# Performance work log

Measured on AMD Instinct MI355X. Metric: run time of the kernel, lower is better.

Reference implementation:

```python
import jax, jax.numpy as jnp
import numpy as np

EPS = 1e-8
ELASTICITY = jnp.array([0.05, 0.12, 0.08, 0.15, 0.10], dtype=jnp.float32)
N_SIDE = 3  # sqrt(control_points=9)


def _kernel_distance(d2):
    # kornia TPS radial basis: 0.5 * r^2 * log(r^2 + eps)
    return 0.5 * d2 * jnp.log(d2 + EPS)


def _pair_sq_dist(a, b):  # [B,N,2],[B,M,2] -> [B,N,M]
    return jnp.sum((a[:, :, None, :] - b[:, None, :, :]) ** 2, axis=-1)


def grid_sample_bilinear(img, grid):
    """F.grid_sample, mode=bilinear, padding_mode=zeros, align_corners=True.
    img [B,C,H,W], grid [B,H,W,2] with (x,y) in [-1,1]."""
    B, C, H, W = img.shape
    gx = (grid[..., 0] + 1.0) * 0.5 * (W - 1)
    gy = (grid[..., 1] + 1.0) * 0.5 * (H - 1)
    x0 = jnp.floor(gx); y0 = jnp.floor(gy)
    x1 = x0 + 1.0; y1 = y0 + 1.0
    wx1 = gx - x0; wx0 = 1.0 - wx1
    wy1 = gy - y0; wy0 = 1.0 - wy1
    b = jnp.arange(B)[:, None, None]

    def gather(yi, xi):
        valid = (xi >= 0) & (xi <= W - 1) & (yi >= 0) & (yi <= H - 1)
        xc = jnp.clip(xi, 0, W - 1).astype(jnp.int32)
        yc = jnp.clip(yi, 0, H - 1).astype(jnp.int32)
        v = img[b, :, yc, xc]  # [B,H,W,C]
        return v * valid[..., None].astype(img.dtype)

    out = (gather(y0, x0) * (wy0 * wx0)[..., None]
           + gather(y0, x1) * (wy0 * wx1)[..., None]
           + gather(y1, x0) * (wy1 * wx0)[..., None]
           + gather(y1, x1) * (wy1 * wx1)[..., None])
    return jnp.transpose(out, (0, 3, 1, 2))


def control_points_src(B):
    ii, jj = jnp.meshgrid(jnp.arange(N_SIDE, dtype=jnp.float32),
                          jnp.arange(N_SIDE, dtype=jnp.float32), indexing='ij')
    src = jnp.stack([2.0 * ii / (N_SIDE - 1) - 1.0,
                     2.0 * jj / (N_SIDE - 1) - 1.0], axis=-1).reshape(-1, 2)
    return jnp.broadcast_to(src, (B, N_SIDE * N_SIDE, 2))


def point_elasticity(masks_f):
    # masks_f [B,nc,H,W]; 5x5 window around each control point, argmax class
    H, W = masks_f.shape[2], masks_f.shape[3]
    elas = []
    for i in range(N_SIDE):
        for j in range(N_SIDE):
            y = int(i / (N_SIDE - 1) * (H - 1))
            x = int(j / (N_SIDE - 1) * (W - 1))
            y0, y1 = max(0, y - 2), min(H, y + 3)
            x0, x1 = max(0, x - 2), min(W, x + 3)
            region = masks_f[:, :, y0:y1, x0:x1].sum((2, 3))  # [B,nc]
            dom = jnp.argmax(region, axis=1)
            elas.append(ELASTICITY[dom])
    return jnp.stack(elas, axis=1)  # [B,9]


def get_tps_transform(src, dst):
    B, N, _ = src.shape
    K = _kernel_distance(_pair_sq_dist(src, src))                 # [B,N,N]
    P = jnp.concatenate([jnp.ones((B, N, 1), src.dtype), src], -1)  # [B,N,3]
    top = jnp.concatenate([K, P], axis=-1)
    bot = jnp.concatenate([jnp.swapaxes(P, 1, 2),
                           jnp.zeros((B, 3, 3), src.dtype)], axis=-1)
    L = jnp.concatenate([top, bot], axis=1)                        # [B,N+3,N+3]
    rhs = jnp.concatenate([dst, jnp.zeros((B, 3, 2), src.dtype)], axis=1)
    w = jnp.linalg.solve(L, rhs)
    return w[:, :N], w[:, N:]


def warp_image_tps(img, centers, kernel_w, affine_w):
    B, C, H, W = img.shape
    gx, gy = jnp.meshgrid(jnp.linspace(-1.0, 1.0, W), jnp.linspace(-1.0, 1.0, H))
    pts = jnp.stack([gx.ravel(), gy.ravel()], axis=-1)             # [HW,2]
    pts = jnp.broadcast_to(pts, (B, H * W, 2))
    k = _kernel_distance(_pair_sq_dist(pts, centers))              # [B,HW,N]
    pts_aug = jnp.concatenate([jnp.ones((B, H * W, 1), img.dtype), pts], -1)
    warped = k @ kernel_w + pts_aug @ affine_w                     # [B,HW,2]
    return grid_sample_bilinear(img, warped.reshape(B, H, W, 2))


def tps_transform(img, masks_f, noise):
    B = img.shape[0]
    disp = noise * point_elasticity(masks_f)[..., None]            # [B,9,2]
    # smooth the single interior control point (i=j=1 -> idx 4)
    neigh = (disp[:, 1] + disp[:, 7] + disp[:, 3] + disp[:, 5]) * 0.25
    disp = disp.at[:, 4].set(0.8 * disp[:, 4] + 0.2 * neigh)
    src = control_points_src(B)
    kw, aw = get_tps_transform(src, src + disp)
    return warp_image_tps(img, src, kw, aw)


def class_aware_mixup(x, masks_f, lam, perm):
    bg = (masks_f.sum(1, keepdims=True) == 0).astype(x.dtype)
    fg = (masks_f == 1).astype(x.dtype).sum(1, keepdims=True)
    return bg * x + fg * (lam * x + (1.0 - lam) * x[perm])


def setup_inputs() -> dict:
    key = jax.random.key(0)
    k1, k2, k3, k4, k5, k6 = jax.random.split(key, 6)
    B, H, W, NC = 128, 192, 192, 5
    return {
        'x': jax.random.normal(k1, (B, 1, H, W), dtype=jnp.float32),
        'masks': jax.random.randint(k2, (B, NC, H, W), 0, 2, dtype=jnp.int32),
        'lam': jax.random.beta(k3, 0.4, 0.4, dtype=jnp.float32),
        'perm': jax.random.permutation(k4, B).astype(jnp.int32),
        'noise_g': jax.random.normal(k5, (B, 9, 2), dtype=jnp.float32),
        'noise_l': jax.random.normal(k6, (B, 9, 2), dtype=jnp.float32),
        'epoch': 10,
        'total_epochs': 100,
    }


def reference(x, masks, lam, perm, noise_g, noise_l, epoch, total_epochs):
    masks_f = masks.astype(x.dtype)
    mixed_x = class_aware_mixup(x, masks_f, lam, perm)
    global_aug = tps_transform(mixed_x, masks_f, noise_g)
    local_aug = tps_transform(x, masks_f, noise_l)
    return (global_aug, local_aug)
```

## Files before the change

kernel.cpp:

```cpp
#include <hip/hip_runtime.h>
#include <math.h>

#define B_    128
#define H_    192
#define W_    192
#define NC_   5
#define HW_   (H_*W_)
#define NPTS  9
#define EPS_  1e-8f
#define CHUNK 8
#define MIXB  (B_*HW_/4/256)
#define LOCB  ((W_/64)*(H_/4)*(B_/CHUNK))

typedef int   vint4   __attribute__((ext_vector_type(4)));
typedef float vfloat4 __attribute__((ext_vector_type(4)));
typedef float vfloat2 __attribute__((ext_vector_type(2)));

struct LinvT { float m[12][NPTS]; };

__global__ void prep_kernel(const int* __restrict__ masks,
                            const float* __restrict__ ng,
                            const float* __restrict__ nl,
                            LinvT Linv, float* __restrict__ wts)
{
    const float ETAB[5] = {0.05f, 0.12f, 0.08f, 0.15f, 0.1f};
    __shared__ int   sums[NPTS][NC_];
    __shared__ float elas_s[NPTS];
    int b = blockIdx.x;
    int t = threadIdx.x;

    if (t < NPTS * NC_) {
        int pt = t / NC_, c = t - pt * NC_;
        int i = pt / 3, j = pt % 3;
        int yc = (i * (H_ - 1)) / 2;
        int xc = (j * (W_ - 1)) / 2;
        int y0 = yc - 2 < 0 ? 0 : yc - 2;
        int y1 = yc + 3 > H_ ? H_ : yc + 3;
        int x0 = xc - 2 < 0 ? 0 : xc - 2;
        int x1 = xc + 3 > W_ ? W_ : xc + 3;
        int s = 0;
        for (int y = y0; y < y1; ++y)
            for (int xx = x0; xx < x1; ++xx)
                s += masks[((size_t)b * NC_ + c) * HW_ + y * W_ + xx];
        sums[pt][c] = s;
    }
    __syncthreads();
    if (t < NPTS) {
        int best = -1, best_c = 0;
        #pragma unroll
        for (int c = 0; c < NC_; ++c) {
            int s = sums[t][c];
            if (s > best) { best = s; best_c = c; }
        }
        elas_s[t] = ETAB[best_c];
    }
    __syncthreads();
    if (t < 24) {
        int tr = t / 12, r = t - tr * 12;
        const float* noise = (tr == 0) ? ng : nl;
        float disp[NPTS][2];
        #pragma unroll
        for (int k = 0; k < NPTS; ++k) {
            float e = elas_s[k];
            disp[k][0] = noise[((size_t)b * NPTS + k) * 2 + 0] * e;
            disp[k][1] = noise[((size_t)b * NPTS + k) * 2 + 1] * e;
        }
        #pragma unroll
        for (int c = 0; c < 2; ++c) {
            float nb = (disp[1][c] + disp[7][c] + disp[3][c] + disp[5][c]) * 0.25f;
            disp[4][c] = 0.8f * disp[4][c] + 0.2f * nb;
        }
        float a0 = 0.f, a1 = 0.f;
        #pragma unroll
        for (int k = 0; k < NPTS; ++k) {
            float d0 = (float)(k / 3 - 1) + disp[k][0];
            float d1 = (float)(k % 3 - 1) + disp[k][1];
            a0 += Linv.m[r][k] * d0;
            a1 += Linv.m[r][k] * d1;
        }
        float* wout = wts + ((size_t)tr * B_ + b) * 24;
        wout[r * 2 + 0] = a0;
        wout[r * 2 + 1] = a1;
    }
}

__device__ __forceinline__ void tps_coords_pk(
    const vfloat2* __restrict__ wt2, float px, float py, const float* __restrict__ u,
    int& o00, int& o01, int& o10, int& o11,
    float& w00, float& w01, float& w10, float& w11)
{
    vfloat2 g = wt2[9];
    g = __builtin_elementwise_fma((vfloat2){px, px}, wt2[10], g);
    g = __builtin_elementwise_fma((vfloat2){py, py}, wt2[11], g);
    #pragma unroll
    for (int k = 0; k < NPTS; ++k)
        g = __builtin_elementwise_fma((vfloat2){u[k], u[k]}, wt2[k], g);
    const float sc = 0.5f * (float)(W_ - 1);
    float ix = fmaf(g.x, sc, sc);
    float iy = fmaf(g.y, sc, sc);
    float x0f = floorf(ix), y0f = floorf(iy);
    float wx1 = ix - x0f, wx0 = 1.f - wx1;
    float wy1 = iy - y0f, wy0 = 1.f - wy1;
    int x0 = (int)x0f, y0 = (int)y0f;
    float fx0 = ((unsigned)x0 < 192u)       ? wx0 : 0.f;
    float fx1 = ((unsigned)(x0 + 1) < 192u) ? wx1 : 0.f;
    float fy0 = ((unsigned)y0 < 192u)       ? wy0 : 0.f;
    float fy1 = ((unsigned)(y0 + 1) < 192u) ? wy1 : 0.f;
    w00 = fy0 * fx0; w01 = fy0 * fx1; w10 = fy1 * fx0; w11 = fy1 * fx1;
    int o = y0 * W_ + x0;
    o00 = min(max(o, 0), HW_ - 1);
    o01 = min(max(o + 1, 0), HW_ - 1);
    o10 = min(max(o + W_, 0), HW_ - 1);
    o11 = min(max(o + W_ + 1, 0), HW_ - 1);
}

__device__ __forceinline__ void warp_body(
    const float* __restrict__ srcb, const float* __restrict__ wts,
    float* __restrict__ out, int gx, int gy, int combo0)
{
    int tx  = threadIdx.x;
    int wpx = gx * 64 + (tx & 63);
    int h   = gy * 4 + (tx >> 6);
    int p   = h * W_ + wpx;
    float px = -1.f + wpx * (2.f / (float)(W_ - 1));
    float py = -1.f + h   * (2.f / (float)(H_ - 1));

    float u[NPTS];
    #pragma unroll
    for (int k = 0; k < NPTS; ++k) {
        float dx = px - (float)(k / 3 - 1);
        float dy = py - (float)(k % 3 - 1);
        float d2 = dx * dx + dy * dy;
        u[k] = 0.5f * d2 * __logf(d2 + EPS_);
    }

    const vfloat2* wt2base = reinterpret_cast<const vfloat2*>(wts);

    #pragma unroll
    for (int g4 = 0; g4 < CHUNK; g4 += 4) {
        int   o00[4], o01[4], o10[4], o11[4];
        float w00[4], w01[4], w10[4], w11[4];
        const float* src[4];
        #pragma unroll
        for (int q = 0; q < 4; ++q) {
            int combo = combo0 + g4 + q;
            int b = combo & (B_ - 1);
            src[q] = srcb + (size_t)b * HW_;
            tps_coords_pk(wt2base + (size_t)combo * 12, px, py, u,
                          o00[q], o01[q], o10[q], o11[q],
                          w00[q], w01[q], w10[q], w11[q]);
        }
        float v00[4], v01[4], v10[4], v11[4];
        #pragma unroll
        for (int q = 0; q < 4; ++q) {
            v00[q] = src[q][o00[q]];
            v01[q] = src[q][o01[q]];
            v10[q] = src[q][o10[q]];
            v11[q] = src[q][o11[q]];
        }
        #pragma unroll
        for (int q = 0; q < 4; ++q) {
            int combo = combo0 + g4 + q;
            float val = w00[q] * v00[q] + w01[q] * v01[q] +
                        w10[q] * v10[q] + w11[q] * v11[q];
            __builtin_nontemporal_store(val, &out[(size_t)combo * HW_ + p]);
        }
    }
}

__global__ __launch_bounds__(256, 2) void mix_local_kernel(
    const float* __restrict__ x, const int* __restrict__ masks,
    const float* __restrict__ lam_p, const int* __restrict__ perm,
    float* __restrict__ mixed, const float* __restrict__ wts,
    float* __restrict__ out)
{
    int bid   = blockIdx.x;
    int group = bid / 3;
    int r     = bid - group * 3;

    if (r < 2) {
        int mb  = group * 2 + r;
        int idx = mb * 256 + threadIdx.x;
        float lam = lam_p[0];
        int b  = idx / (HW_ / 4);
        int p4 = (idx - b * (HW_ / 4)) * 4;
        const vfloat4 xv = *reinterpret_cast<const vfloat4*>(x + (size_t)b * HW_ + p4);
        int pb = perm[b];
        const vfloat4 xp = *reinterpret_cast<const vfloat4*>(x + (size_t)pb * HW_ + p4);

        vint4 ma[NC_];
        #pragma unroll
        for (int c = 0; c < NC_; ++c)
            ma[c] = __builtin_nontemporal_load(
                reinterpret_cast<const vint4*>(masks + ((size_t)b * NC_ + c) * HW_ + p4));
        vfloat4 outv;
        #pragma unroll
        for (int l = 0; l < 4; ++l) {
            int s = 0, fg = 0;
            #pragma unroll
            for (int c = 0; c < NC_; ++c) { int m = ma[c][l]; s += m; fg += (m == 1); }
            float bg = (s == 0) ? 1.f : 0.f;
            outv[l] = bg * xv[l] + (float)fg * (lam * xv[l] + (1.f - lam) * xp[l]);
        }
        *reinterpret_cast<vfloat4*>(mixed + (size_t)b * HW_ + p4) = outv;
    } else {
        int lb = group;
        int gx = lb % 3;
        int gy = (lb / 3) % 48;
        int gz = lb / 144;
        warp_body(x, wts, out, gx, gy, B_ + gz * CHUNK);
    }
}

__global__ __launch_bounds__(256, 2) void warp_global_kernel(
    const float* __restrict__ mixed, const float* __restrict__ wts,
    float* __restrict__ out)
{
    warp_body(mixed, wts, out, blockIdx.x, blockIdx.y, blockIdx.z * CHUNK);
}

static void build_linv(LinvT* out)
{
    double srcp[NPTS][2];
    for (int k = 0; k < NPTS; ++k) {
        srcp[k][0] = (double)(k / 3) - 1.0;
        srcp[k][1] = (double)(k % 3) - 1.0;
    }
    double A[12][24];
    for (int r = 0; r < 12; ++r)
        for (int c = 0; c < 24; ++c) A[r][c] = 0.0;
    for (int i = 0; i < NPTS; ++i) {
        for (int j = 0; j < NPTS; ++j) {
            double dx = srcp[i][0] - srcp[j][0];
            double dy = srcp[i][1] - srcp[j][1];
            double d2 = dx * dx + dy * dy;
            A[i][j] = 0.5 * d2 * log(d2 + 1e-8);
        }
        A[i][9]  = 1.0; A[i][10] = srcp[i][0]; A[i][11] = srcp[i][1];
        A[9][i]  = 1.0; A[10][i] = srcp[i][0]; A[11][i] = srcp[i][1];
    }
    for (int r = 0; r < 12; ++r) A[r][12 + r] = 1.0;
    for (int col = 0; col < 12; ++col) {
        int piv = col; double mx = fabs(A[col][col]);
        for (int r = col + 1; r < 12; ++r)
            if (fabs(A[r][col]) > mx) { mx = fabs(A[r][col]); piv = r; }
        if (piv != col)
            for (int c = 0; c < 24; ++c) { double tmp = A[col][c]; A[col][c] = A[piv][c]; A[piv][c] = tmp; }
        double d = A[col][col];
        for (int c = 0; c < 24; ++c) A[col][c] /= d;
        for (int r = 0; r < 12; ++r) {
            if (r == col) continue;
            double f = A[r][col];
            if (f != 0.0)
                for (int c = 0; c < 24; ++c) A[r][c] -= f * A[col][c];
        }
    }
    for (int r = 0; r < 12; ++r)
        for (int k = 0; k < NPTS; ++k)
            out->m[r][k] = (float)A[r][12 + k];
}

extern "C" void kernel_launch(void* const* d_in, const int* in_sizes, int n_in,
                              void* d_out, int out_size, void* d_ws, size_t ws_size,
                              hipStream_t stream)
{
    (void)in_sizes; (void)n_in; (void)out_size; (void)ws_size;
    const float* x     = (const float*)d_in[0];
    const int*   masks = (const int*)d_in[1];
    const float* lam   = (const float*)d_in[2];
    const int*   perm  = (const int*)d_in[3];
    const float* ng    = (const float*)d_in[4];
    const float* nl    = (const float*)d_in[5];
    float* out = (float*)d_out;

    char* ws = (char*)d_ws;
    float* wts   = (float*)ws;
    float* mixed = (float*)(ws + 32768);

    LinvT Linv;
    build_linv(&Linv);

    prep_kernel<<<B_, 64, 0, stream>>>(masks, ng, nl, Linv, wts);
    mix_local_kernel<<<MIXB + LOCB, 256, 0, stream>>>(
        x, masks, lam, perm, mixed, wts, out);
    warp_global_kernel<<<dim3(W_ / 64, H_ / 4, (B_ / CHUNK)), 256, 0, stream>>>(
        mixed, wts, out);
}
```

Before: 58.62 us.

## Split mixup and warps into three staged kernels to overlap global warp

```diff
diff --git a/kernel.cpp b/kernel.cpp
--- a/kernel.cpp
+++ b/kernel.cpp
@@ -9,8 +9,8 @@
 #define NPTS  9
 #define EPS_  1e-8f
 #define CHUNK 8
-#define MIXB  (B_*HW_/4/256)
-#define LOCB  ((W_/64)*(H_/4)*(B_/CHUNK))
+#define MIXBH 2304
+#define LOCBH 1152
 
 typedef int   vint4   __attribute__((ext_vector_type(4)));
 typedef float vfloat4 __attribute__((ext_vector_type(4)));
@@ -168,7 +168,37 @@
     }
 }
 
-__global__ __launch_bounds__(256, 2) void mix_local_kernel(
+__device__ __forceinline__ void mixup_body(
+    const float* __restrict__ x, const int* __restrict__ masks,
+    const float* __restrict__ lam_p, const int* __restrict__ perm,
+    float* __restrict__ mixed, int mb)
+{
+    int idx = mb * 256 + threadIdx.x;
+    float lam = lam_p[0];
+    int b  = idx / (HW_ / 4);
+    int p4 = (idx - b * (HW_ / 4)) * 4;
+    const vfloat4 xv = *reinterpret_cast<const vfloat4*>(x + (size_t)b * HW_ + p4);
+    int pb = perm[b];
+    const vfloat4 xp = *reinterpret_cast<const vfloat4*>(x + (size_t)pb * HW_ + p4);
+
+    vint4 ma[NC_];
+    #pragma unroll
+    for (int c = 0; c < NC_; ++c)
+        ma[c] = __builtin_nontemporal_load(
+            reinterpret_cast<const vint4*>(masks + ((size_t)b * NC_ + c) * HW_ + p4));
+    vfloat4 outv;
+    #pragma unroll
+    for (int l = 0; l < 4; ++l) {
+        int s = 0, fg = 0;
+        #pragma unroll
+        for (int c = 0; c < NC_; ++c) { int m = ma[c][l]; s += m; fg += (m == 1); }
+        float bg = (s == 0) ? 1.f : 0.f;
+        outv[l] = bg * xv[l] + (float)fg * (lam * xv[l] + (1.f - lam) * xp[l]);
+    }
+    *reinterpret_cast<vfloat4*>(mixed + (size_t)b * HW_ + p4) = outv;
+}
+
+__global__ __launch_bounds__(256, 2) void half_a_kernel(
     const float* __restrict__ x, const int* __restrict__ masks,
     const float* __restrict__ lam_p, const int* __restrict__ perm,
     float* __restrict__ mixed, const float* __restrict__ wts,
@@ -177,46 +207,42 @@
     int bid   = blockIdx.x;
     int group = bid / 3;
     int r     = bid - group * 3;
-
     if (r < 2) {
-        int mb  = group * 2 + r;
-        int idx = mb * 256 + threadIdx.x;
-        float lam = lam_p[0];
-        int b  = idx / (HW_ / 4);
-        int p4 = (idx - b * (HW_ / 4)) * 4;
-        const vfloat4 xv = *reinterpret_cast<const vfloat4*>(x + (size_t)b * HW_ + p4);
-        int pb = perm[b];
-        const vfloat4 xp = *reinterpret_cast<const vfloat4*>(x + (size_t)pb * HW_ + p4);
-
-        vint4 ma[NC_];
-        #pragma unroll
-        for (int c = 0; c < NC_; ++c)
-            ma[c] = __builtin_nontemporal_load(
-                reinterpret_cast<const vint4*>(masks + ((size_t)b * NC_ + c) * HW_ + p4));
-        vfloat4 outv;
-        #pragma unroll
-        for (int l = 0; l < 4; ++l) {
-            int s = 0, fg = 0;
-            #pragma unroll
-            for (int c = 0; c < NC_; ++c) { int m = ma[c][l]; s += m; fg += (m == 1); }
-            float bg = (s == 0) ? 1.f : 0.f;
-            outv[l] = bg * xv[l] + (float)fg * (lam * xv[l] + (1.f - lam) * xp[l]);
-        }
-        *reinterpret_cast<vfloat4*>(mixed + (size_t)b * HW_ + p4) = outv;
+        mixup_body(x, masks, lam_p, perm, mixed, group * 2 + r);
     } else {
         int lb = group;
-        int gx = lb % 3;
-        int gy = (lb / 3) % 48;
-        int gz = lb / 144;
+        int gx = lb % 3, gy = (lb / 3) % 48, gz = lb / 144;
         warp_body(x, wts, out, gx, gy, B_ + gz * CHUNK);
     }
 }
 
-__global__ __launch_bounds__(256, 2) void warp_global_kernel(
+__global__ __launch_bounds__(256, 2) void half_b_kernel(
+    const float* __restrict__ x, const int* __restrict__ masks,
+    const float* __restrict__ lam_p, const int* __restrict__ perm,
+    float* __restrict__ mixed, const float* __restrict__ wts,
+    float* __restrict__ out)
+{
+    int bid   = blockIdx.x;
+    int group = bid / 4;
+    int r     = bid - group * 4;
+    if (r < 2) {
+        mixup_body(x, masks, lam_p, perm, mixed, MIXBH + group * 2 + r);
+    } else if (r == 2) {
+        int lb = group;
+        int gx = lb % 3, gy = (lb / 3) % 48, gz = lb / 144;
+        warp_body(x, wts, out, gx, gy, B_ + 64 + gz * CHUNK);
+    } else {
+        int lb = group;
+        int gx = lb % 3, gy = (lb / 3) % 48, gz = lb / 144;
+        warp_body(mixed, wts, out, gx, gy, gz * CHUNK);
+    }
+}
+
+__global__ __launch_bounds__(256, 2) void half_c_kernel(
     const float* __restrict__ mixed, const float* __restrict__ wts,
     float* __restrict__ out)
 {
-    warp_body(mixed, wts, out, blockIdx.x, blockIdx.y, blockIdx.z * CHUNK);
+    warp_body(mixed, wts, out, blockIdx.x, blockIdx.y, 64 + blockIdx.z * CHUNK);
 }
 
 static void build_linv(LinvT* out)
@@ -281,8 +307,9 @@
     build_linv(&Linv);
 
     prep_kernel<<<B_, 64, 0, stream>>>(masks, ng, nl, Linv, wts);
-    mix_local_kernel<<<MIXB + LOCB, 256, 0, stream>>>(
+    half_a_kernel<<<MIXBH + LOCBH, 256, 0, stream>>>(
         x, masks, lam, perm, mixed, wts, out);
-    warp_global_kernel<<<dim3(W_ / 64, H_ / 4, (B_ / CHUNK)), 256, 0, stream>>>(
-        mixed, wts, out);
-}
+    half_b_kernel<<<MIXBH + 2 * LOCBH, 256, 0, stream>>>(
+        x, masks, lam, perm, mixed, wts, out);
+    half_c_kernel<<<dim3(3, 48, 8), 256, 0, stream>>>(mixed, wts, out);
+}
```

Measured after the change: 66.10 us. 12.8% more time.
